# Performance work log

Measured on AMD Instinct MI355X. Metric: run time of the kernel, lower is better.

Reference implementation:

```python
import jax, jax.numpy as jnp
import numpy as np

N = 50000
E = 1600000
D_IN, D_H1, D_H2 = 256, 128, 64


def setup_inputs() -> dict:
    key = jax.random.key(0)
    ks = jax.random.split(key, 16)
    def lin(k, fan_in, fan_out):
        # torch nn.Linear default init: U(-1/sqrt(fan_in), 1/sqrt(fan_in))
        kw, kb = jax.random.split(k)
        bound = 1.0 / np.sqrt(fan_in)
        W = jax.random.uniform(kw, (fan_out, fan_in), jnp.float32, -bound, bound)
        b = jax.random.uniform(kb, (fan_out,), jnp.float32, -bound, bound)
        return W, b
    x = jax.random.normal(ks[0], (N, D_IN), jnp.float32)
    edge_index = jax.random.randint(ks[1], (2, E), 0, N, jnp.int64)
    edge_weight = jax.random.uniform(ks[2], (E,), jnp.float32)
    enc1_w, enc1_b = lin(ks[3], D_IN, D_H1)
    enc2_w, enc2_b = lin(ks[4], D_H1, D_H2)
    gcn1_w, gcn1_b = lin(ks[5], D_H2, D_H2)
    gcn2_w, gcn2_b = lin(ks[6], D_H2, D_H2)
    dec1_w, dec1_b = lin(ks[7], D_H2, D_H1)
    dec2_w, dec2_b = lin(ks[8], D_H1, D_IN)
    return dict(x=x, edge_index=edge_index, edge_weight=edge_weight,
                enc1_w=enc1_w, enc1_b=enc1_b, enc2_w=enc2_w, enc2_b=enc2_b,
                gcn1_w=gcn1_w, gcn1_b=gcn1_b, gcn2_w=gcn2_w, gcn2_b=gcn2_b,
                dec1_w=dec1_w, dec1_b=dec1_b, dec2_w=dec2_w, dec2_b=dec2_b)


def _gcn_conv(h, src, dst, w_all, W, b, n_nodes):
    # PyG GCNConv: h' = D^{-1/2}(A+I)D^{-1/2} (h W^T) + b; self-loops already in src/dst/w_all
    h = h @ W.T
    deg = jax.ops.segment_sum(w_all, dst, num_segments=n_nodes)
    dinv = jnp.where(deg > 0, jax.lax.rsqrt(jnp.maximum(deg, 1e-12)), 0.0)
    norm = dinv[src] * w_all * dinv[dst]                 # [E+N]
    msg = h[src] * norm[:, None]                         # gather + scale
    out = jax.ops.segment_sum(msg, dst, num_segments=n_nodes)  # scatter-add
    return out + b


def reference(x, edge_index, edge_weight,
              enc1_w, enc1_b, enc2_w, enc2_b,
              gcn1_w, gcn1_b, gcn2_w, gcn2_b,
              dec1_w, dec1_b, dec2_w, dec2_b):
    n = x.shape[0]
    # add self-loops (weight 1.0), as PyG GCNConv does by default
    loop = jnp.arange(n, dtype=edge_index.dtype)
    src = jnp.concatenate([edge_index[0], loop])
    dst = jnp.concatenate([edge_index[1], loop])
    w_all = jnp.concatenate([edge_weight, jnp.ones((n,), edge_weight.dtype)])

    h = jax.nn.relu(x @ enc1_w.T + enc1_b)
    h = jax.nn.relu(h @ enc2_w.T + enc2_b)
    h = jax.nn.relu(_gcn_conv(h, src, dst, w_all, gcn1_w, gcn1_b, n))
    h = jax.nn.relu(_gcn_conv(h, src, dst, w_all, gcn2_w, gcn2_b, n))
    h = jax.nn.relu(h @ dec1_w.T + dec1_b)
    h = h @ dec2_w.T + dec2_b
    return jax.nn.sigmoid(h)
```

## Files before the change

### kernel.cpp

```cpp
#include <hip/hip_runtime.h>


constexpr int NBLK = 128;
constexpr int GRP  = NBLK / 8;

template <int K, int MT, int M, int ACT, bool BIAS>
__global__ __launch_bounds__(256) void gemm_rt(const float* __restrict__ A,
                                               const float* __restrict__ W,
                                               const float* __restrict__ bias,
                                               float* __restrict__ C, int N) {
    constexpr int KC = 16;
    constexpr int NT = 64;
    constexpr int TM = MT / 16;
    constexpr int TN = 4;
    __shared__ float As[KC][NT + 4];
    __shared__ float Ws[KC][MT + 4];

    const int tid  = threadIdx.x;
    const int tx   = tid & 15;
    const int ty   = tid >> 4;
    const int nodeBase = blockIdx.x * NT;
    const int foff     = blockIdx.y * MT;

    float acc[TN][TM];
#pragma unroll
    for (int i = 0; i < TN; ++i)
#pragma unroll
        for (int j = 0; j < TM; ++j) acc[i][j] = 0.f;

    for (int kc = 0; kc < K; kc += KC) {
        __syncthreads();
        {
            int n  = tid >> 2;
            int k4 = tid & 3;
            int gn = nodeBase + n;
            float4 v = make_float4(0.f, 0.f, 0.f, 0.f);
            if (gn < N) v = *(const float4*)(A + (size_t)gn * K + kc + k4 * 4);
            As[k4 * 4 + 0][n] = v.x;
            As[k4 * 4 + 1][n] = v.y;
            As[k4 * 4 + 2][n] = v.z;
            As[k4 * 4 + 3][n] = v.w;
        }
#pragma unroll
        for (int i = 0; i < MT / 64; ++i) {
            int f  = tid + 256 * i;
            int m  = f >> 2;
            int k4 = f & 3;
            float4 v = *(const float4*)(W + (size_t)(foff + m) * K + kc + k4 * 4);
            Ws[k4 * 4 + 0][m] = v.x;
            Ws[k4 * 4 + 1][m] = v.y;
            Ws[k4 * 4 + 2][m] = v.z;
            Ws[k4 * 4 + 3][m] = v.w;
        }
        __syncthreads();
#pragma unroll 4
        for (int k = 0; k < KC; ++k) {
            float a[TN];
            float w[TM];
#pragma unroll
            for (int i = 0; i < TN; ++i) a[i] = As[k][tx + 16 * i];
#pragma unroll
            for (int j4 = 0; j4 < TM / 4; ++j4) {
                float4 wv = *(const float4*)&Ws[k][ty * TM + j4 * 4];
                w[j4 * 4 + 0] = wv.x; w[j4 * 4 + 1] = wv.y;
                w[j4 * 4 + 2] = wv.z; w[j4 * 4 + 3] = wv.w;
            }
#pragma unroll
            for (int i = 0; i < TN; ++i)
#pragma unroll
                for (int j = 0; j < TM; ++j) acc[i][j] = fmaf(a[i], w[j], acc[i][j]);
        }
    }

#pragma unroll
    for (int i = 0; i < TN; ++i) {
        int node = nodeBase + tx + 16 * i;
        if (node < N) {
            float* cp = C + (size_t)node * M + foff + ty * TM;
#pragma unroll
            for (int j4 = 0; j4 < TM / 4; ++j4) {
                float t[4];
#pragma unroll
                for (int c = 0; c < 4; ++c) {
                    float x = acc[i][j4 * 4 + c];
                    if constexpr (BIAS) x += bias[foff + ty * TM + j4 * 4 + c];
                    if constexpr (ACT == 1) x = fmaxf(x, 0.f);
                    if constexpr (ACT == 2) x = 1.f / (1.f + __expf(-x));
                    t[c] = x;
                }
                float4 v; v.x = t[0]; v.y = t[1]; v.z = t[2]; v.w = t[3];
                *(float4*)(cp + j4 * 4) = v;
            }
        }
    }
}


__global__ __launch_bounds__(256) void count_k(const int* __restrict__ ei,
                                               int* __restrict__ cnt,
                                               int NB, int E) {
    __shared__ int hist[784];
    const int tid = threadIdx.x;
    for (int i = tid; i < NB; i += 256) hist[i] = 0;
    __syncthreads();
    const int chunk = (E + NBLK - 1) / NBLK;
    const int lo = blockIdx.x * chunk;
    const int hi = min(lo + chunk, E);
    for (int e = lo + tid; e < hi; e += 256) {
        int d = ei[E + e];
        atomicAdd(&hist[d >> 6], 1);
    }
    __syncthreads();
    const int r = blockIdx.x & 7, g = blockIdx.x >> 3;
    for (int i = tid; i < NB; i += 256)
        cnt[i * NBLK + r * GRP + g] = hist[i];
}

__global__ __launch_bounds__(256) void scan1(const int* __restrict__ cnt,
                                             int* __restrict__ pos,
                                             int* __restrict__ bs, int n) {
    __shared__ int s[256];
    const int t = threadIdx.x;
    const int i0 = blockIdx.x * 512 + 2 * t;
    int c0 = (i0     < n) ? cnt[i0]     : 0;
    int c1 = (i0 + 1 < n) ? cnt[i0 + 1] : 0;
    int c = c0 + c1;
    s[t] = c;
    __syncthreads();
    for (int off = 1; off < 256; off <<= 1) {
        int v = (t >= off) ? s[t - off] : 0;
        __syncthreads();
        s[t] += v;
        __syncthreads();
    }
    int excl = s[t] - c;
    if (i0     < n) pos[i0]     = excl;
    if (i0 + 1 < n) pos[i0 + 1] = excl + c0;
    if (t == 255) bs[blockIdx.x] = s[255];
}

__global__ __launch_bounds__(256) void scan_tops(int* __restrict__ bs, int nb) {
    __shared__ int s[256];
    int t = threadIdx.x;
    int v = (t < nb) ? bs[t] : 0;
    s[t] = v;
    __syncthreads();
    for (int off = 1; off < 256; off <<= 1) {
        int u = (t >= off) ? s[t - off] : 0;
        __syncthreads();
        s[t] += u;
        __syncthreads();
    }
    if (t < nb) bs[t] = s[t] - v;
}

__global__ __launch_bounds__(256) void scan2(int* __restrict__ pos,
                                             const int* __restrict__ bs,
                                             int* __restrict__ bucketBase,
                                             int n, int NB, int E) {
    const int t = threadIdx.x;
    const int i0 = blockIdx.x * 512 + 2 * t;
    const int add = bs[blockIdx.x];
#pragma unroll
    for (int c = 0; c < 2; ++c) {
        int i = i0 + c;
        if (i < n) {
            int v = pos[i] + add;
            pos[i] = v;
            if ((i & (NBLK - 1)) == 0) bucketBase[i >> 7] = v;
        }
    }
    if (blockIdx.x == 0 && t == 0) bucketBase[NB] = E;
}

__global__ __launch_bounds__(256) void place_k(const int* __restrict__ ei,
                                               const float* __restrict__ w,
                                               const int* __restrict__ pos,
                                               int2* __restrict__ ebuf,
                                               int NB, int E) {
    __shared__ int cur[784];
    const int tid = threadIdx.x;
    const int r = blockIdx.x & 7, g = blockIdx.x >> 3;
    for (int i = tid; i < NB; i += 256) cur[i] = pos[i * NBLK + r * GRP + g];
    __syncthreads();
    const int chunk = (E + NBLK - 1) / NBLK;
    const int lo = blockIdx.x * chunk;
    const int hi = min(lo + chunk, E);
    for (int e = lo + tid; e < hi; e += 256) {
        int s = ei[e];
        int d = ei[E + e];
        float wv = w[e];
        int p = atomicAdd(&cur[d >> 6], 1);
        ebuf[p] = make_int2(s | ((d & 63) << 26), __float_as_int(wv));
    }
}

__global__ __launch_bounds__(256) void bucket_build(const int2* __restrict__ ebuf,
                                                    const int* __restrict__ bucketBase,
                                                    int2* __restrict__ sn,
                                                    int* __restrict__ row,
                                                    float* __restrict__ dinv,
                                                    int N, int E) {
    __shared__ int   lh[64];
    __shared__ float ldg[64];
    __shared__ int   sc[64];
    __shared__ int   lofs[64];
    const int tid  = threadIdx.x;
    const int base = bucketBase[blockIdx.x];
    const int end  = bucketBase[blockIdx.x + 1];

    if (tid < 64) { lh[tid] = 0; ldg[tid] = 0.f; }
    __syncthreads();
    for (int i = base + tid; i < end; i += 256) {
        int2 v = ebuf[i];
        int dl = ((unsigned)v.x) >> 26;
        atomicAdd(&lh[dl], 1);
        atomicAdd(&ldg[dl], __int_as_float(v.y));
    }
    __syncthreads();
    if (tid < 64) sc[tid] = lh[tid];
    __syncthreads();
    for (int off = 1; off < 64; off <<= 1) {
        int v = (tid < 64 && tid >= off) ? sc[tid - off] : 0;
        __syncthreads();
        if (tid < 64) sc[tid] += v;
        __syncthreads();
    }
    if (tid < 64) {
        int excl = sc[tid] - lh[tid];
        int d = (blockIdx.x << 6) + tid;
        if (d < N) {
            row[d]  = base + excl;
            dinv[d] = rsqrtf(fmaxf(1.0f + ldg[tid], 1e-12f));
        }
        lofs[tid] = base + excl;
    }
    __syncthreads();
    for (int i = base + tid; i < end; i += 256) {
        int2 v = ebuf[i];
        unsigned u = (unsigned)v.x;
        int dl = u >> 26;
        int s  = u & 0x03FFFFFF;
        int p  = atomicAdd(&lofs[dl], 1);
        sn[p] = make_int2(s, v.y);
    }
    if (blockIdx.x == 0 && tid == 0) row[N] = E;
}

__global__ __launch_bounds__(256) void scale_pay(int2* __restrict__ sn,
                                                 const float* __restrict__ dinv,
                                                 int E) {
    int p = blockIdx.x * 256 + threadIdx.x;
    if (p < E) {
        int2 v = sn[p];
        sn[p] = make_int2(v.x, __float_as_int(__int_as_float(v.y) * dinv[v.x]));
    }
}

__global__ __launch_bounds__(256) void gcn_agg(const float* __restrict__ t,
                                               const int2* __restrict__ sn,
                                               const int* __restrict__ row,
                                               const float* __restrict__ dinv,
                                               const float* __restrict__ bias,
                                               float* __restrict__ out, int N) {
    const int lane = threadIdx.x & 63;
    int i = __builtin_amdgcn_readfirstlane((int)(blockIdx.x * 4) + (threadIdx.x >> 6));
    if (i >= N) return;
    float di   = dinv[i];
    float self = t[(size_t)i * 64 + lane];
    float acc  = 0.f;
    int p  = row[i];
    int pe = row[i + 1];
    for (; p + 4 <= pe; p += 4) {
        int2 v0 = sn[p];
        int2 v1 = sn[p + 1];
        int2 v2 = sn[p + 2];
        int2 v3 = sn[p + 3];
        acc += t[(size_t)v0.x * 64 + lane] * __int_as_float(v0.y);
        acc += t[(size_t)v1.x * 64 + lane] * __int_as_float(v1.y);
        acc += t[(size_t)v2.x * 64 + lane] * __int_as_float(v2.y);
        acc += t[(size_t)v3.x * 64 + lane] * __int_as_float(v3.y);
    }
    for (; p < pe; ++p) {
        int2 v = sn[p];
        acc += t[(size_t)v.x * 64 + lane] * __int_as_float(v.y);
    }
    float x = (acc + self * di) * di + bias[lane];
    out[(size_t)i * 64 + lane] = fmaxf(x, 0.f);
}

extern "C" void kernel_launch(void* const* d_in, const int* in_sizes, int n_in,
                              void* d_out, int out_size, void* d_ws, size_t ws_size,
                              hipStream_t stream) {
    const float* x      = (const float*)d_in[0];
    const int*   ei     = (const int*)d_in[1];
    const float* ew     = (const float*)d_in[2];
    const float* enc1_w = (const float*)d_in[3];
    const float* enc1_b = (const float*)d_in[4];
    const float* enc2_w = (const float*)d_in[5];
    const float* enc2_b = (const float*)d_in[6];
    const float* gcn1_w = (const float*)d_in[7];
    const float* gcn1_b = (const float*)d_in[8];
    const float* gcn2_w = (const float*)d_in[9];
    const float* gcn2_b = (const float*)d_in[10];
    const float* dec1_w = (const float*)d_in[11];
    const float* dec1_b = (const float*)d_in[12];
    const float* dec2_w = (const float*)d_in[13];
    const float* dec2_b = (const float*)d_in[14];

    const int N  = in_sizes[0] / 256;
    const int E  = in_sizes[2];
    const int NB = (N + 63) / 64;
    const int NCNT = NB * NBLK;
    const int NS   = (NCNT + 511) / 512;

    float* ws   = (float*)d_ws;
    float* bufA = ws;
    int2*  sn   = (int2*)bufA;
    float* bufC = bufA + (size_t)2 * E;
    int2*  ebuf = (int2*)bufC;
    float* bufB = bufA + (size_t)N * 128;
    float* dinv = bufB + (size_t)N * 64;
    int*   row  = (int*)(dinv + N);
    int*   cnt  = row + (N + 1);
    int*   pos  = cnt + NCNT;
    int*   bucketBase = pos + NCNT;
    int*   bs   = bucketBase + (NB + 1);

    const int gemmGrid = (N + 63) / 64;
    const int nBlkE    = (E + 255) / 256;

    gemm_rt<256, 128, 128, 1, true><<<dim3(gemmGrid, 1), 256, 0, stream>>>(
        x, enc1_w, enc1_b, bufA, N);
    gemm_rt<128, 64, 64, 1, true><<<dim3(gemmGrid, 1), 256, 0, stream>>>(
        bufA, enc2_w, enc2_b, bufB, N);

    count_k<<<NBLK, 256, 0, stream>>>(ei, cnt, NB, E);
    scan1<<<NS, 256, 0, stream>>>(cnt, pos, bs, NCNT);
    scan_tops<<<1, 256, 0, stream>>>(bs, NS);
    scan2<<<NS, 256, 0, stream>>>(pos, bs, bucketBase, NCNT, NB, E);
    place_k<<<NBLK, 256, 0, stream>>>(ei, ew, pos, ebuf, NB, E);
    bucket_build<<<NB, 256, 0, stream>>>(ebuf, bucketBase, sn, row, dinv, N, E);
    scale_pay<<<nBlkE, 256, 0, stream>>>(sn, dinv, E);

    gemm_rt<64, 64, 64, 0, false><<<dim3(gemmGrid, 1), 256, 0, stream>>>(
        bufB, gcn1_w, nullptr, bufC, N);
    gcn_agg<<<(N + 3) / 4, 256, 0, stream>>>(bufC, sn, row, dinv, gcn1_b, bufB, N);

    gemm_rt<64, 64, 64, 0, false><<<dim3(gemmGrid, 1), 256, 0, stream>>>(
        bufB, gcn2_w, nullptr, bufC, N);
    gcn_agg<<<(N + 3) / 4, 256, 0, stream>>>(bufC, sn, row, dinv, gcn2_b, bufB, N);

    gemm_rt<64, 128, 128, 1, true><<<dim3(gemmGrid, 1), 256, 0, stream>>>(
        bufB, dec1_w, dec1_b, bufA, N);
    gemm_rt<128, 128, 256, 2, true><<<dim3(gemmGrid, 2), 256, 0, stream>>>(
        bufA, dec2_w, dec2_b, (float*)d_out, N);
}
```

Before: 506.6 us.

## Replace FP32 SIMT GEMMs with split-bf16 MFMA GEMMs

Replaces the scalar FMA tiled GEMM with a matrix-core kernel. Each fp32 operand is split into high and low bf16 parts, and three MFMA 16x16x32 products (hi*hi, lo*hi, hi*lo) approximate fp32 accuracy. The kernel uses 128x64 tiles with register prefetch of the next K chunk, and the launch grids change to match. The aim is to move the six dense layers from vector ALU to matrix cores. In exchange it adds split and LDS conversion overhead, uses scalar (non-vectorized) output stores, and carries a small precision change.

```diff
diff --git a/kernel.cpp b/kernel.cpp
--- a/kernel.cpp
+++ b/kernel.cpp
@@ -4,92 +4,147 @@
 constexpr int NBLK = 128;
 constexpr int GRP  = NBLK / 8;
 
-template <int K, int MT, int M, int ACT, bool BIAS>
-__global__ __launch_bounds__(256) void gemm_rt(const float* __restrict__ A,
+typedef __attribute__((ext_vector_type(8))) short bf16x8;
+typedef __attribute__((ext_vector_type(4))) float f32x4;
+
+__device__ inline void split2(float f0, float f1, unsigned& hp, unsigned& lp) {
+    unsigned u0 = __float_as_uint(f0), u1 = __float_as_uint(f1);
+    hp = (u1 & 0xFFFF0000u) | (u0 >> 16);
+    float r0 = f0 - __uint_as_float(u0 & 0xFFFF0000u);
+    float r1 = f1 - __uint_as_float(u1 & 0xFFFF0000u);
+    lp = (__float_as_uint(r1) & 0xFFFF0000u) | (__float_as_uint(r0) >> 16);
+}
+
+template <int K, int M, int ACT, bool BIAS>
+__global__ __launch_bounds__(256) void gemm_mf(const float* __restrict__ A,
                                                const float* __restrict__ W,
                                                const float* __restrict__ bias,
                                                float* __restrict__ C, int N) {
-    constexpr int KC = 16;
-    constexpr int NT = 64;
-    constexpr int TM = MT / 16;
-    constexpr int TN = 4;
-    __shared__ float As[KC][NT + 4];
-    __shared__ float Ws[KC][MT + 4];
-
-    const int tid  = threadIdx.x;
-    const int tx   = tid & 15;
-    const int ty   = tid >> 4;
-    const int nodeBase = blockIdx.x * NT;
-    const int foff     = blockIdx.y * MT;
-
-    float acc[TN][TM];
-#pragma unroll
-    for (int i = 0; i < TN; ++i)
-#pragma unroll
-        for (int j = 0; j < TM; ++j) acc[i][j] = 0.f;
+    static_assert(K % 64 == 0, "K%64");
+    constexpr int KC = 64;
+    __shared__ unsigned Ah[128][36];
+    __shared__ unsigned Al[128][36];
+    __shared__ unsigned Wh[64][36];
+    __shared__ unsigned Wl[64][36];
+
+    const int tid      = threadIdx.x;
+    const int nodeBase = blockIdx.x * 128;
+    const int foff     = blockIdx.y * 64;
+
+    const int srow = tid >> 4;
+    const int sc4  = tid & 15;
+    float4 av[8];
+    float4 wv[4];
+
+#pragma unroll
+    for (int q = 0; q < 8; ++q) {
+        const int r  = q * 16 + srow;
+        const int gn = nodeBase + r;
+        av[q] = (gn < N) ? *(const float4*)(A + (size_t)gn * K + sc4 * 4)
+                         : make_float4(0.f, 0.f, 0.f, 0.f);
+    }
+#pragma unroll
+    for (int q = 0; q < 4; ++q) {
+        const int r = q * 16 + srow;
+        wv[q] = *(const float4*)(W + (size_t)(foff + r) * K + sc4 * 4);
+    }
+
+    f32x4 acc[4][2];
+#pragma unroll
+    for (int mf = 0; mf < 4; ++mf)
+#pragma unroll
+        for (int nf = 0; nf < 2; ++nf) acc[mf][nf] = (f32x4)0.f;
+
+    const int lane = tid & 63;
+    const int wid  = tid >> 6;
+    const int wm   = wid >> 1;
+    const int wn   = wid & 1;
+    const int fr   = lane & 15;
+    const int fg   = lane >> 4;
 
     for (int kc = 0; kc < K; kc += KC) {
-        __syncthreads();
-        {
-            int n  = tid >> 2;
-            int k4 = tid & 3;
-            int gn = nodeBase + n;
-            float4 v = make_float4(0.f, 0.f, 0.f, 0.f);
-            if (gn < N) v = *(const float4*)(A + (size_t)gn * K + kc + k4 * 4);
-            As[k4 * 4 + 0][n] = v.x;
-            As[k4 * 4 + 1][n] = v.y;
-            As[k4 * 4 + 2][n] = v.z;
-            As[k4 * 4 + 3][n] = v.w;
-        }
-#pragma unroll
-        for (int i = 0; i < MT / 64; ++i) {
-            int f  = tid + 256 * i;
-            int m  = f >> 2;
-            int k4 = f & 3;
-            float4 v = *(const float4*)(W + (size_t)(foff + m) * K + kc + k4 * 4);
-            Ws[k4 * 4 + 0][m] = v.x;
-            Ws[k4 * 4 + 1][m] = v.y;
-            Ws[k4 * 4 + 2][m] = v.z;
-            Ws[k4 * 4 + 3][m] = v.w;
-        }
-        __syncthreads();
-#pragma unroll 4
-        for (int k = 0; k < KC; ++k) {
-            float a[TN];
-            float w[TM];
-#pragma unroll
-            for (int i = 0; i < TN; ++i) a[i] = As[k][tx + 16 * i];
-#pragma unroll
-            for (int j4 = 0; j4 < TM / 4; ++j4) {
-                float4 wv = *(const float4*)&Ws[k][ty * TM + j4 * 4];
-                w[j4 * 4 + 0] = wv.x; w[j4 * 4 + 1] = wv.y;
-                w[j4 * 4 + 2] = wv.z; w[j4 * 4 + 3] = wv.w;
+#pragma unroll
+        for (int q = 0; q < 8; ++q) {
+            unsigned h0, l0, h1, l1;
+            split2(av[q].x, av[q].y, h0, l0);
+            split2(av[q].z, av[q].w, h1, l1);
+            const int r = q * 16 + srow;
+            Ah[r][sc4 * 2] = h0; Ah[r][sc4 * 2 + 1] = h1;
+            Al[r][sc4 * 2] = l0; Al[r][sc4 * 2 + 1] = l1;
+        }
+#pragma unroll
+        for (int q = 0; q < 4; ++q) {
+            unsigned h0, l0, h1, l1;
+            split2(wv[q].x, wv[q].y, h0, l0);
+            split2(wv[q].z, wv[q].w, h1, l1);
+            const int r = q * 16 + srow;
+            Wh[r][sc4 * 2] = h0; Wh[r][sc4 * 2 + 1] = h1;
+            Wl[r][sc4 * 2] = l0; Wl[r][sc4 * 2 + 1] = l1;
+        }
+        __syncthreads();
+
+        if (kc + KC < K) {
+#pragma unroll
+            for (int q = 0; q < 8; ++q) {
+                const int r  = q * 16 + srow;
+                const int gn = nodeBase + r;
+                av[q] = (gn < N)
+                    ? *(const float4*)(A + (size_t)gn * K + kc + KC + sc4 * 4)
+                    : make_float4(0.f, 0.f, 0.f, 0.f);
             }
 #pragma unroll
-            for (int i = 0; i < TN; ++i)
-#pragma unroll
-                for (int j = 0; j < TM; ++j) acc[i][j] = fmaf(a[i], w[j], acc[i][j]);
-        }
-    }
-
-#pragma unroll
-    for (int i = 0; i < TN; ++i) {
-        int node = nodeBase + tx + 16 * i;
-        if (node < N) {
-            float* cp = C + (size_t)node * M + foff + ty * TM;
-#pragma unroll
-            for (int j4 = 0; j4 < TM / 4; ++j4) {
-                float t[4];
-#pragma unroll
-                for (int c = 0; c < 4; ++c) {
-                    float x = acc[i][j4 * 4 + c];
-                    if constexpr (BIAS) x += bias[foff + ty * TM + j4 * 4 + c];
+            for (int q = 0; q < 4; ++q) {
+                const int r = q * 16 + srow;
+                wv[q] = *(const float4*)(W + (size_t)(foff + r) * K + kc + KC + sc4 * 4);
+            }
+        }
+
+#pragma unroll
+        for (int kf = 0; kf < 2; ++kf) {
+            bf16x8 ah[4], alo[4], bh[2], blo[2];
+#pragma unroll
+            for (int mf = 0; mf < 4; ++mf) {
+                const int r = wm * 64 + mf * 16 + fr;
+                ah[mf]  = *(const bf16x8*)&Ah[r][kf * 16 + fg * 4];
+                alo[mf] = *(const bf16x8*)&Al[r][kf * 16 + fg * 4];
+            }
+#pragma unroll
+            for (int nf = 0; nf < 2; ++nf) {
+                const int r = wn * 32 + nf * 16 + fr;
+                bh[nf]  = *(const bf16x8*)&Wh[r][kf * 16 + fg * 4];
+                blo[nf] = *(const bf16x8*)&Wl[r][kf * 16 + fg * 4];
+            }
+#pragma unroll
+            for (int mf = 0; mf < 4; ++mf)
+#pragma unroll
+                for (int nf = 0; nf < 2; ++nf) {
+                    acc[mf][nf] = __builtin_amdgcn_mfma_f32_16x16x32_bf16(
+                        ah[mf], bh[nf], acc[mf][nf], 0, 0, 0);
+                    acc[mf][nf] = __builtin_amdgcn_mfma_f32_16x16x32_bf16(
+                        alo[mf], bh[nf], acc[mf][nf], 0, 0, 0);
+                    acc[mf][nf] = __builtin_amdgcn_mfma_f32_16x16x32_bf16(
+                        ah[mf], blo[nf], acc[mf][nf], 0, 0, 0);
+                }
+        }
+        __syncthreads();
+    }
+
+#pragma unroll
+    for (int nf = 0; nf < 2; ++nf) {
+        const int feat = foff + wn * 32 + nf * 16 + fr;
+        const float bv = BIAS ? bias[feat] : 0.f;
+#pragma unroll
+        for (int mf = 0; mf < 4; ++mf) {
+            const int node0 = nodeBase + wm * 64 + mf * 16 + fg * 4;
+#pragma unroll
+            for (int i = 0; i < 4; ++i) {
+                const int node = node0 + i;
+                if (node < N) {
+                    float x = acc[mf][nf][i] + bv;
                     if constexpr (ACT == 1) x = fmaxf(x, 0.f);
                     if constexpr (ACT == 2) x = 1.f / (1.f + __expf(-x));
-                    t[c] = x;
+                    C[(size_t)node * M + feat] = x;
                 }
-                float4 v; v.x = t[0]; v.y = t[1]; v.z = t[2]; v.w = t[3];
-                *(float4*)(cp + j4 * 4) = v;
             }
         }
     }
@@ -327,12 +382,12 @@
     int*   bucketBase = pos + NCNT;
     int*   bs   = bucketBase + (NB + 1);
 
-    const int gemmGrid = (N + 63) / 64;
+    const int gemmGrid = (N + 127) / 128;
     const int nBlkE    = (E + 255) / 256;
 
-    gemm_rt<256, 128, 128, 1, true><<<dim3(gemmGrid, 1), 256, 0, stream>>>(
+    gemm_mf<256, 128, 1, true><<<dim3(gemmGrid, 2), 256, 0, stream>>>(
         x, enc1_w, enc1_b, bufA, N);
-    gemm_rt<128, 64, 64, 1, true><<<dim3(gemmGrid, 1), 256, 0, stream>>>(
+    gemm_mf<128, 64, 1, true><<<dim3(gemmGrid, 1), 256, 0, stream>>>(
         bufA, enc2_w, enc2_b, bufB, N);
 
     count_k<<<NBLK, 256, 0, stream>>>(ei, cnt, NB, E);
@@ -343,16 +398,16 @@
     bucket_build<<<NB, 256, 0, stream>>>(ebuf, bucketBase, sn, row, dinv, N, E);
     scale_pay<<<nBlkE, 256, 0, stream>>>(sn, dinv, E);
 
-    gemm_rt<64, 64, 64, 0, false><<<dim3(gemmGrid, 1), 256, 0, stream>>>(
+    gemm_mf<64, 64, 0, false><<<dim3(gemmGrid, 1), 256, 0, stream>>>(
         bufB, gcn1_w, nullptr, bufC, N);
     gcn_agg<<<(N + 3) / 4, 256, 0, stream>>>(bufC, sn, row, dinv, gcn1_b, bufB, N);
 
-    gemm_rt<64, 64, 64, 0, false><<<dim3(gemmGrid, 1), 256, 0, stream>>>(
+    gemm_mf<64, 64, 0, false><<<dim3(gemmGrid, 1), 256, 0, stream>>>(
         bufB, gcn2_w, nullptr, bufC, N);
     gcn_agg<<<(N + 3) / 4, 256, 0, stream>>>(bufC, sn, row, dinv, gcn2_b, bufB, N);
 
-    gemm_rt<64, 128, 128, 1, true><<<dim3(gemmGrid, 1), 256, 0, stream>>>(
+    gemm_mf<64, 128, 1, true><<<dim3(gemmGrid, 2), 256, 0, stream>>>(
         bufB, dec1_w, dec1_b, bufA, N);
-    gemm_rt<128, 128, 256, 2, true><<<dim3(gemmGrid, 2), 256, 0, stream>>>(
+    gemm_mf<128, 256, 2, true><<<dim3(gemmGrid, 4), 256, 0, stream>>>(
         bufA, dec2_w, dec2_b, (float*)d_out, N);
 }
```

Result: faster. 462.1 us (-8.8%).
